# Kernel optimization log

Hardware: AMD Instinct MI355X
Metric: run time of the kernel (lower is better)

## Reference

```python
import jax, jax.numpy as jnp
import numpy as np

B, L, S, H, E, D = 2, 2048, 2048, 16, 64, 64

def setup_inputs() -> dict:
    key = jax.random.key(0)
    kq, kk, kv = jax.random.split(key, 3)
    queries = jax.random.normal(kq, (B, L, H, E), dtype=jnp.float32)
    keys = jax.random.normal(kk, (B, S, H, E), dtype=jnp.float32)
    values = jax.random.normal(kv, (B, S, H, D), dtype=jnp.float32)
    # TriangularCausalMask: True above the diagonal (masked positions)
    causal = jnp.triu(jnp.ones((L, S), dtype=bool), k=1)
    attn_mask = jnp.broadcast_to(causal[None, None], (B, 1, L, S))
    z = jnp.zeros((1,), dtype=jnp.float32)
    return {"queries": queries, "keys": keys, "values": values,
            "query_omegas": z, "query_thetas": z, "key_omegas": z,
            "key_thetas": z, "attn_mask": attn_mask}

def reference(queries, keys, values, query_omegas, query_thetas,
              key_omegas, key_thetas, attn_mask):
    # omegas/thetas are unused in FullAttention.forward (kept for signature parity)
    scale = 1.0 / jnp.sqrt(jnp.float32(E))
    scores = jnp.einsum('blhe,bshe->bhls', queries, keys)  # [B,H,L,S]
    scores = jnp.where(attn_mask, -jnp.inf, scores)
    A = jax.nn.softmax(scale * scores, axis=-1)  # dropout p=0 (eval)
    V = jnp.einsum('bhls,bshd->blhd', A, values)
    return V
```

## Files before the change

kernel.cpp:

```cpp
#include <hip/hip_runtime.h>
#include <hip/hip_bf16.h>
#include <math.h>

typedef __attribute__((ext_vector_type(8))) short bf16x8;
typedef __attribute__((ext_vector_type(16))) float f32x16;

#define B_ 2
#define L_ 2048
#define S_ 2048
#define H_ 16
#define E_ 64
#define D_ 64
#define EXP2(x) exp2f(x)

#define KOFF 0ull
#define VOFF (8ull << 20)
#define POFF (16ull << 20)
#define SLOT_BYTES 18432ull
#define NSLOTS 1120ull
#define WS_NEED (POFF + NSLOTS * SLOT_BYTES)

#define GLL(gp, lp) __builtin_amdgcn_global_load_lds( \
    (const __attribute__((address_space(1))) unsigned int*)(gp), \
    (__attribute__((address_space(3))) unsigned int*)(lp), 16, 0, 0)

__device__ __forceinline__ unsigned pkbf(float a, float b) {
  __hip_bfloat162 hh = __float22bfloat162_rn(float2{a, b});
  return *(unsigned*)&hh;
}
__device__ __forceinline__ float bf2f(unsigned us) {
  return __uint_as_float(us << 16);
}
__device__ __forceinline__ int crow(int r, int hi5) {
  return (r & 3) + ((r >> 2) << 3) + (hi5 << 2);
}
__device__ __forceinline__ int nchunks(int q) { return (q >= 10) ? 3 : ((q >= 3) ? 2 : 1); }
__device__ __forceinline__ int slotoff(int q, int c) {
  return (q < 3) ? q : (q < 10) ? 3 + (q - 3) * 2 + c : 17 + (q - 10) * 3 + c;
}

__global__ __launch_bounds__(256)
void fa_pre(const float* __restrict__ Kp, const float* __restrict__ Vp,
            char* __restrict__ ws) {
  const int Bx = blockIdx.x;
  const int bh = Bx & 31, t = Bx >> 5;
  const int b = bh >> 4, h = bh & 15;
  const int kv0 = t * 64;
  const int tid = threadIdx.x;
  char* dk = ws + KOFF + ((size_t)(bh * 32 + t)) * 8192;
  char* dv = ws + VOFF + ((size_t)(bh * 32 + t)) * 8192;
  const int krow = tid >> 2, ksg = tid & 3;
  const int kswz = (krow & 7) << 4;
  const float* gk = Kp + ((size_t)(b * S_ + kv0 + krow) * H_ + h) * E_ + ksg * 16;
  float4 a0 = ((const float4*)gk)[0], a1 = ((const float4*)gk)[1];
  float4 a2 = ((const float4*)gk)[2], a3 = ((const float4*)gk)[3];
  uint4 u0{pkbf(a0.x, a0.y), pkbf(a0.z, a0.w), pkbf(a1.x, a1.y), pkbf(a1.z, a1.w)};
  uint4 u1{pkbf(a2.x, a2.y), pkbf(a2.z, a2.w), pkbf(a3.x, a3.y), pkbf(a3.z, a3.w)};
  *(uint4*)(dk + ((krow * 128 + ksg * 32) ^ kswz)) = u0;
  *(uint4*)(dk + ((krow * 128 + ksg * 32 + 16) ^ kswz)) = u1;
  const int vd = tid & 63, kg = tid >> 6;
  const int vswz = (vd & 7) << 4;
  const float* gv = Vp + ((size_t)(b * S_ + kv0 + kg * 16) * H_ + h) * D_ + vd;
  float v[16];
  #pragma unroll
  for (int k = 0; k < 16; ++k) v[k] = gv[(size_t)k * (H_ * D_)];
  uint4 w0{pkbf(v[0], v[1]), pkbf(v[2], v[3]), pkbf(v[4], v[5]), pkbf(v[6], v[7])};
  uint4 w1{pkbf(v[8], v[9]), pkbf(v[10], v[11]), pkbf(v[12], v[13]), pkbf(v[14], v[15])};
  *(uint4*)(dv + ((vd * 128 + kg * 32) ^ vswz)) = w0;
  *(uint4*)(dv + ((vd * 128 + kg * 32 + 16) ^ vswz)) = w1;
}

__global__ __launch_bounds__(256, 3)
void fa_main(const float* __restrict__ Qp, char* __restrict__ ws) {
  __shared__ uint4 sbuf[2][1024];

  const int tid  = threadIdx.x;
  const int lane = tid & 63;
  const int sub  = tid >> 6;
  const int l31  = lane & 31;
  const int hi5  = lane >> 5;

  const int Bx  = blockIdx.x;
  const int xcd = Bx & 7, i_ = Bx >> 3;
  const int bh  = xcd * 4 + (i_ & 3);
  const int j   = i_ >> 2;
  int q, c;
  if (j < 18)      { q = 15 - j / 3;       c = j % 3; }
  else if (j < 32) { q = 9 - (j - 18) / 2; c = (j - 18) & 1; }
  else             { q = 34 - j;           c = 0; }
  const int b = bh >> 4, h = bh & 15;
  const int tot = 2 * q + 2, nc = nchunks(q);
  const int base = tot / nc, rem = tot - base * nc;
  const int R  = base + (c < rem ? 1 : 0);
  const int t0 = c * base + (c < rem ? c : rem);
  const int q0 = q << 7;
  const int qw = q0 + sub * 32;

  const float cs = 0.125f * 1.44269504088896f;

  bf16x8 qf[4];
  {
    const int qg = qw + l31;
    const float* gq = Qp + ((size_t)(b * L_ + qg) * H_ + h) * E_ + hi5 * 8;
    #pragma unroll
    for (int ec = 0; ec < 4; ++ec) {
      float4 a = *(const float4*)(gq + ec * 16);
      float4 cc = *(const float4*)(gq + ec * 16 + 4);
      uint4 u;
      u.x = pkbf(a.x * cs, a.y * cs);
      u.y = pkbf(a.z * cs, a.w * cs);
      u.z = pkbf(cc.x * cs, cc.y * cs);
      u.w = pkbf(cc.z * cs, cc.w * cs);
      qf[ec] = *(bf16x8*)&u;
    }
  }

  f32x16 acc[2];
  #pragma unroll
  for (int dt = 0; dt < 2; ++dt)
    #pragma unroll
    for (int rr = 0; rr < 16; ++rr) acc[dt][rr] = 0.f;
  float mrun = -INFINITY, lsum = 0.f;

  const char* gK = ws + KOFF + ((size_t)bh * 32) * 8192;
  const char* gV = ws + VOFF + ((size_t)bh * 32) * 8192;

#define STAGE(buf_, t_) do {                                        \
    const char* sk = gK + (size_t)(t_) * 8192 + tid * 16;           \
    const char* sv = gV + (size_t)(t_) * 8192 + tid * 16;           \
    char* lb = (char*)&sbuf[(buf_)][0] + tid * 16;                  \
    GLL(sk, lb); GLL(sk + 4096, lb + 4096);                         \
    GLL(sv, lb + 8192); GLL(sv + 4096, lb + 12288);                 \
  } while (0)

  STAGE(0, t0);
  __syncthreads();

  int cur = 0;
  for (int t = t0; t < t0 + R; ++t, cur ^= 1) {
    if (t + 1 < t0 + R) STAGE(cur ^ 1, t + 1);

    const int kv0 = t * 64;
    if (kv0 <= qw + 31) {
      char* lk = (char*)&sbuf[cur][0];
      char* lv = lk + 8192;
      const bool needmask = (kv0 + 63) > qw;

      f32x16 st[2];
      #pragma unroll
      for (int c2 = 0; c2 < 2; ++c2)
        #pragma unroll
        for (int rr = 0; rr < 16; ++rr) st[c2][rr] = 0.f;
      __builtin_amdgcn_s_setprio(1);
      #pragma unroll
      for (int c2 = 0; c2 < 2; ++c2) {
        const int row = c2 * 32 + l31;
        const int sw = (row & 7) << 4;
        #pragma unroll
        for (int ec = 0; ec < 4; ++ec) {
          bf16x8 kf = *(bf16x8*)(lk + ((row * 128 + ec * 32 + hi5 * 16) ^ sw));
          st[c2] = __builtin_amdgcn_mfma_f32_32x32x16_bf16(kf, qf[ec], st[c2], 0, 0, 0);
        }
      }
      __builtin_amdgcn_s_setprio(0);

      if (needmask) {
        const int qg = qw + l31;
        #pragma unroll
        for (int c2 = 0; c2 < 2; ++c2)
          #pragma unroll
          for (int rr = 0; rr < 16; ++rr)
            if (kv0 + c2 * 32 + crow(rr, hi5) > qg) st[c2][rr] = -1e30f;
      }

      float pm = st[0][0];
      #pragma unroll
      for (int c2 = 0; c2 < 2; ++c2)
        #pragma unroll
        for (int rr = 0; rr < 16; ++rr) pm = fmaxf(pm, st[c2][rr]);
      pm = fmaxf(pm, __shfl_xor(pm, 32));

      if (__any(pm > mrun + 8.f)) {
        const float mn = fmaxf(mrun, pm);
        const float f = EXP2(mrun - mn);
        mrun = mn;
        lsum *= f;
        #pragma unroll
        for (int rr = 0; rr < 16; ++rr) {
          const float fr = __shfl(f, crow(rr, hi5));
          acc[0][rr] *= fr;
          acc[1][rr] *= fr;
        }
      }
      {
        float ps = 0.f;
        #pragma unroll
        for (int c2 = 0; c2 < 2; ++c2)
          #pragma unroll
          for (int rr = 0; rr < 16; ++rr) {
            st[c2][rr] = EXP2(st[c2][rr] - mrun);
            ps += st[c2][rr];
          }
        ps += __shfl_xor(ps, 32);
        lsum += ps;
      }

      uint4 pa[4];
      #pragma unroll
      for (int c2 = 0; c2 < 2; ++c2) {
        unsigned Dw[8];
        #pragma unroll
        for (int jj = 0; jj < 8; ++jj)
          Dw[jj] = pkbf(st[c2][2 * jj], st[c2][2 * jj + 1]);
        unsigned y0 = __shfl_xor((int)(hi5 ? Dw[0] : Dw[2]), 32);
        unsigned y1 = __shfl_xor((int)(hi5 ? Dw[1] : Dw[3]), 32);
        unsigned y2 = __shfl_xor((int)(hi5 ? Dw[4] : Dw[6]), 32);
        unsigned y3 = __shfl_xor((int)(hi5 ? Dw[5] : Dw[7]), 32);
        uint4 p0, p1;
        if (hi5) {
          p0 = uint4{y0, y1, Dw[2], Dw[3]};
          p1 = uint4{y2, y3, Dw[6], Dw[7]};
        } else {
          p0 = uint4{Dw[0], Dw[1], y0, y1};
          p1 = uint4{Dw[4], Dw[5], y2, y3};
        }
        pa[2 * c2]     = p0;
        pa[2 * c2 + 1] = p1;
      }

      __builtin_amdgcn_s_setprio(1);
      #pragma unroll
      for (int s = 0; s < 4; ++s) {
        #pragma unroll
        for (int dt = 0; dt < 2; ++dt) {
          const int row = dt * 32 + l31;
          bf16x8 vf = *(bf16x8*)(lv + ((row * 128 + s * 32 + hi5 * 16) ^ ((row & 7) << 4)));
          acc[dt] = __builtin_amdgcn_mfma_f32_32x32x16_bf16(*(bf16x8*)&pa[s], vf, acc[dt], 0, 0, 0);
        }
      }
      __builtin_amdgcn_s_setprio(0);
    }
    __syncthreads();
  }

  char* slot = ws + POFF + ((size_t)(bh * 35 + slotoff(q, c))) * SLOT_BYTES;
  uint4* pw = (uint4*)(slot + (size_t)(sub * 64 + lane) * 64);
  #pragma unroll
  for (int dt = 0; dt < 2; ++dt) {
    uint4 A{pkbf(acc[dt][0], acc[dt][1]),  pkbf(acc[dt][2], acc[dt][3]),
            pkbf(acc[dt][4], acc[dt][5]),  pkbf(acc[dt][6], acc[dt][7])};
    uint4 Bq{pkbf(acc[dt][8], acc[dt][9]),  pkbf(acc[dt][10], acc[dt][11]),
             pkbf(acc[dt][12], acc[dt][13]), pkbf(acc[dt][14], acc[dt][15])};
    pw[dt * 2]     = A;
    pw[dt * 2 + 1] = Bq;
  }
  ((float2*)(slot + 16384))[sub * 64 + lane] = float2{mrun, lsum};
#undef STAGE
}

__device__ __forceinline__ void unpk(uint4 a, uint4 b, float* o) {
  const unsigned* pa = (const unsigned*)&a;
  const unsigned* pb = (const unsigned*)&b;
  #pragma unroll
  for (int i = 0; i < 4; ++i) {
    o[2 * i]     = bf2f(pa[i] & 0xffffu);
    o[2 * i + 1] = bf2f(pa[i] >> 16);
    o[8 + 2 * i]     = bf2f(pb[i] & 0xffffu);
    o[8 + 2 * i + 1] = bf2f(pb[i] >> 16);
  }
}

__global__ __launch_bounds__(256)
void fa_merge(float* __restrict__ Op, const char* __restrict__ ws) {
  const int Bx = blockIdx.x;
  const int bh = Bx >> 4, q = Bx & 15;
  const int b = bh >> 4, h = bh & 15;
  const int tid = threadIdx.x, lane = tid & 63, sub = tid >> 6;
  const int l31 = lane & 31, hi5 = lane >> 5;
  const int nc = nchunks(q);
  const char* sbase = ws + POFF;

  float A0[16], A1[16], M, Lw;
  {
    const char* s0 = sbase + ((size_t)(bh * 35 + slotoff(q, 0))) * SLOT_BYTES;
    const uint4* pr = (const uint4*)(s0 + (size_t)(sub * 64 + lane) * 64);
    unpk(pr[0], pr[1], A0);
    unpk(pr[2], pr[3], A1);
    float2 ml = ((const float2*)(s0 + 16384))[sub * 64 + lane];
    M = ml.x; Lw = ml.y;
  }
  for (int ci = 1; ci < nc; ++ci) {
    const char* si = sbase + ((size_t)(bh * 35 + slotoff(q, ci))) * SLOT_BYTES;
    const uint4* pr = (const uint4*)(si + (size_t)(sub * 64 + lane) * 64);
    float a0[16], a1[16];
    unpk(pr[0], pr[1], a0);
    unpk(pr[2], pr[3], a1);
    float2 ml = ((const float2*)(si + 16384))[sub * 64 + lane];
    const float mm = fmaxf(M, ml.x);
    const float fA = EXP2(M - mm);
    const float fI = EXP2(ml.x - mm);
    Lw = Lw * fA + ml.y * fI;
    M = mm;
    #pragma unroll
    for (int rr = 0; rr < 16; ++rr) {
      const int cr = crow(rr, hi5);
      const float fAb = __shfl(fA, cr);
      const float fIb = __shfl(fI, cr);
      A0[rr] = A0[rr] * fAb + a0[rr] * fIb;
      A1[rr] = A1[rr] * fAb + a1[rr] * fIb;
    }
  }
  const float inv = 1.f / Lw;
  #pragma unroll
  for (int rr = 0; rr < 16; ++rr) {
    const int cr = crow(rr, hi5);
    const float wv = __shfl(inv, cr);
    const int qg = (q << 7) + sub * 32 + cr;
    float* go = Op + ((size_t)(b * L_ + qg) * H_ + h) * D_ + l31;
    go[0]  = A0[rr] * wv;
    go[32] = A1[rr] * wv;
  }
}

extern "C" void kernel_launch(void* const* d_in, const int* in_sizes, int n_in,
                              void* d_out, int out_size, void* d_ws, size_t ws_size,
                              hipStream_t stream) {
  (void)in_sizes; (void)n_in; (void)out_size; (void)ws_size;
  const float* Q = (const float*)d_in[0];
  const float* K = (const float*)d_in[1];
  const float* V = (const float*)d_in[2];
  float* O = (float*)d_out;
  char* ws = (char*)d_ws;
  fa_pre<<<dim3(1024), dim3(256), 0, stream>>>(K, V, ws);
  fa_main<<<dim3(1120), dim3(256), 0, stream>>>(Q, ws);
  fa_merge<<<dim3(512), dim3(256), 0, stream>>>(O, ws);
}
```

Baseline: 63.83 us.

## Write single-chunk query tiles directly from main kernel and tree-reduce softmax stats

Query tiles that are processed as a single KV chunk (q<3) now normalize and write the output directly in fa_main, skipping the workspace round-trip. The merge kernel launches only for tiles with multiple chunks. The row max and row sum reductions are rewritten as balanced trees to shorten dependency chains, and launch bounds raise the occupancy target from 3 to 4 blocks. The higher occupancy target may force register spilling.

Measured after the change: 64.68 us. About the same (+1.3%).

```diff
diff --git a/kernel.cpp b/kernel.cpp
--- a/kernel.cpp
+++ b/kernel.cpp
@@ -70,8 +70,9 @@
   *(uint4*)(dv + ((vd * 128 + kg * 32 + 16) ^ vswz)) = w1;
 }
 
-__global__ __launch_bounds__(256, 3)
-void fa_main(const float* __restrict__ Qp, char* __restrict__ ws) {
+__global__ __launch_bounds__(256, 4)
+void fa_main(const float* __restrict__ Qp, float* __restrict__ Op,
+             char* __restrict__ ws) {
   __shared__ uint4 sbuf[2][1024];
 
   const int tid  = threadIdx.x;
@@ -173,11 +174,16 @@
             if (kv0 + c2 * 32 + crow(rr, hi5) > qg) st[c2][rr] = -1e30f;
       }
 
-      float pm = st[0][0];
-      #pragma unroll
-      for (int c2 = 0; c2 < 2; ++c2)
-        #pragma unroll
-        for (int rr = 0; rr < 16; ++rr) pm = fmaxf(pm, st[c2][rr]);
+      float mx[8];
+      #pragma unroll
+      for (int i = 0; i < 8; ++i)
+        mx[i] = fmaxf(fmaxf(st[0][i], st[0][i + 8]),
+                      fmaxf(st[1][i], st[1][i + 8]));
+      #pragma unroll
+      for (int i = 0; i < 4; ++i) mx[i] = fmaxf(mx[i], mx[i + 4]);
+      mx[0] = fmaxf(mx[0], mx[2]);
+      mx[1] = fmaxf(mx[1], mx[3]);
+      float pm = fmaxf(mx[0], mx[1]);
       pm = fmaxf(pm, __shfl_xor(pm, 32));
 
       if (__any(pm > mrun + 8.f)) {
@@ -193,14 +199,18 @@
         }
       }
       {
-        float ps = 0.f;
         #pragma unroll
         for (int c2 = 0; c2 < 2; ++c2)
           #pragma unroll
-          for (int rr = 0; rr < 16; ++rr) {
+          for (int rr = 0; rr < 16; ++rr)
             st[c2][rr] = EXP2(st[c2][rr] - mrun);
-            ps += st[c2][rr];
-          }
+        float ss[8];
+        #pragma unroll
+        for (int i = 0; i < 8; ++i)
+          ss[i] = (st[0][i] + st[0][i + 8]) + (st[1][i] + st[1][i + 8]);
+        #pragma unroll
+        for (int i = 0; i < 4; ++i) ss[i] += ss[i + 4];
+        float ps = (ss[0] + ss[2]) + (ss[1] + ss[3]);
         ps += __shfl_xor(ps, 32);
         lsum += ps;
       }
@@ -243,6 +253,20 @@
     __syncthreads();
   }
 
+  if (nc == 1) {
+    const float inv = 1.f / lsum;
+    #pragma unroll
+    for (int rr = 0; rr < 16; ++rr) {
+      const int cr = crow(rr, hi5);
+      const float wv = __shfl(inv, cr);
+      const int qg = qw + cr;
+      float* go = Op + ((size_t)(b * L_ + qg) * H_ + h) * D_ + l31;
+      go[0]  = acc[0][rr] * wv;
+      go[32] = acc[1][rr] * wv;
+    }
+    return;
+  }
+
   char* slot = ws + POFF + ((size_t)(bh * 35 + slotoff(q, c))) * SLOT_BYTES;
   uint4* pw = (uint4*)(slot + (size_t)(sub * 64 + lane) * 64);
   #pragma unroll
@@ -273,7 +297,7 @@
 __global__ __launch_bounds__(256)
 void fa_merge(float* __restrict__ Op, const char* __restrict__ ws) {
   const int Bx = blockIdx.x;
-  const int bh = Bx >> 4, q = Bx & 15;
+  const int bh = Bx / 13, q = 3 + (Bx % 13);
   const int b = bh >> 4, h = bh & 15;
   const int tid = threadIdx.x, lane = tid & 63, sub = tid >> 6;
   const int l31 = lane & 31, hi5 = lane >> 5;
@@ -332,6 +356,6 @@
   float* O = (float*)d_out;
   char* ws = (char*)d_ws;
   fa_pre<<<dim3(1024), dim3(256), 0, stream>>>(K, V, ws);
-  fa_main<<<dim3(1120), dim3(256), 0, stream>>>(Q, ws);
-  fa_merge<<<dim3(512), dim3(256), 0, stream>>>(O, ws);
-}
+  fa_main<<<dim3(1120), dim3(256), 0, stream>>>(Q, O, ws);
+  fa_merge<<<dim3(416), dim3(256), 0, stream>>>(O, ws);
+}
```
